# Performance work log

Hardware: AMD Instinct MI355X
Metric: run time of the kernel (lower is better)

## Reference

```python
import jax, jax.numpy as jnp
import numpy as np

EMB = 768
HEADS = 12
HEAD_DIM = EMB // HEADS


def setup_inputs() -> dict:
    key = jax.random.key(0)
    ks = jax.random.split(key, 9)
    B, L, D = 4, 2048, EMB
    s = 1.0 / np.sqrt(D)
    return {
        "x": jax.random.normal(ks[0], (B, L, D), dtype=jnp.float32),
        "Wq": jax.random.normal(ks[1], (D, D), dtype=jnp.float32) * s,
        "bq": jnp.zeros((D,), dtype=jnp.float32),
        "Wk": jax.random.normal(ks[2], (D, D), dtype=jnp.float32) * s,
        "bk": jnp.zeros((D,), dtype=jnp.float32),
        "Wv": jax.random.normal(ks[3], (D, D), dtype=jnp.float32) * s,
        "bv": jnp.zeros((D,), dtype=jnp.float32),
        "Wo": jax.random.normal(ks[4], (D, D), dtype=jnp.float32) * s,
        "bo": jnp.zeros((D,), dtype=jnp.float32),
    }


def reference(x, Wq, bq, Wk, bk, Wv, bv, Wo, bo):
    B, L, D = x.shape
    H, hd = HEADS, HEAD_DIM
    # QKV projections -> [B, H, L, hd]
    def proj(W, b):
        return (x @ W + b).reshape(B, L, H, hd).transpose(0, 2, 1, 3)
    Q = proj(Wq, bq)
    K = proj(Wk, bk)
    V = proj(Wv, bv)
    # scores [B, H, L, L]
    scores = jnp.einsum("bhqd,bhkd->bhqk", Q, K) / jnp.sqrt(jnp.float32(hd))
    attn = jax.nn.softmax(scores, axis=-1)
    out = jnp.einsum("bhqk,bhkd->bhqd", attn, V)  # [B,H,L,hd]
    out = out.transpose(0, 2, 1, 3).reshape(B, L, D)
    return out @ Wo + bo
```

## Files before the change

### kernel.cpp

```cpp
#include <hip/hip_runtime.h>
#include <math.h>

#define TL 2048
#define TD 768
#define NH 12
#define HD 64
#define NB 4
#define MTOT (NB * TL)

typedef __bf16 bf16;
typedef __attribute__((ext_vector_type(4))) __bf16 bf16x4;
typedef __attribute__((ext_vector_type(8))) __bf16 bf16x8;
typedef __attribute__((ext_vector_type(4))) float floatx4;

#define QSCALE 0.18033688011112042f

#define MFMA16(A, B, C) __builtin_amdgcn_mfma_f32_16x16x32_bf16(A, B, C, 0, 0, 0)

__device__ __forceinline__ void gl_lds16(const void* g, void* l) {
    __builtin_amdgcn_global_load_lds(
        (const __attribute__((address_space(1))) void*)g,
        (__attribute__((address_space(3))) void*)l, 16, 0, 0);
}

__device__ __forceinline__ floatx4 exp2x4(floatx4 a) {
    floatx4 r;
    r.x = __builtin_amdgcn_exp2f(a.x);
    r.y = __builtin_amdgcn_exp2f(a.y);
    r.z = __builtin_amdgcn_exp2f(a.z);
    r.w = __builtin_amdgcn_exp2f(a.w);
    return r;
}

__device__ __forceinline__ int kperm(int key) {
    return (key & 35) | ((key >> 2) & 1) << 4 | ((key >> 3) & 3) << 2;
}

__global__ __launch_bounds__(256)
void cast_x_kernel(const float* __restrict__ x, bf16* __restrict__ xb)
{
    size_t i = ((size_t)blockIdx.x * 256 + threadIdx.x) * 4;
    float4 v = *(const float4*)(x + i);
    bf16x4 o;
    o[0] = (bf16)v.x; o[1] = (bf16)v.y; o[2] = (bf16)v.z; o[3] = (bf16)v.w;
    *(bf16x4*)(xb + i) = o;
}

__global__ __launch_bounds__(256)
void transw_kernel(const float* __restrict__ W0, const float* __restrict__ W1,
                   const float* __restrict__ W2, const float* __restrict__ W3,
                   bf16* __restrict__ T0, bf16* __restrict__ T1,
                   bf16* __restrict__ T2, bf16* __restrict__ T3)
{
    const int z = blockIdx.z;
    const float* W = z == 0 ? W0 : z == 1 ? W1 : z == 2 ? W2 : W3;
    bf16*       T = z == 0 ? T0 : z == 1 ? T1 : z == 2 ? T2 : T3;
    __shared__ float Ts[64][65];
    const int t = threadIdx.x;
    const int k0 = blockIdx.x * 64, n0 = blockIdx.y * 64;
    const int rr = t >> 4, cc = (t & 15) * 4;
#pragma unroll
    for (int i = 0; i < 4; ++i) {
        int row = rr + i * 16;
        float4 v = *(const float4*)(W + (size_t)(k0 + row) * TD + n0 + cc);
        Ts[row][cc] = v.x; Ts[row][cc + 1] = v.y;
        Ts[row][cc + 2] = v.z; Ts[row][cc + 3] = v.w;
    }
    __syncthreads();
#pragma unroll
    for (int i = 0; i < 4; ++i) {
        int n = rr + i * 16;
        bf16x4 pk;
#pragma unroll
        for (int j = 0; j < 4; ++j) pk[j] = (bf16)Ts[cc + j][n];
        *(bf16x4*)(T + (size_t)(n0 + n) * TD + k0 + cc) = pk;
    }
}

__global__ __launch_bounds__(256)
void qkv_gemm(const bf16* __restrict__ xb,
              const bf16* __restrict__ Wqt, const bf16* __restrict__ Wkt,
              const bf16* __restrict__ Wvt,
              const float* __restrict__ bq, const float* __restrict__ bk,
              const float* __restrict__ bv,
              bf16* __restrict__ Q, bf16* __restrict__ K, bf16* __restrict__ Vt)
{
    __shared__ __align__(16) bf16 As[128 * 32];
    __shared__ __align__(16) bf16 Bs[128 * 32];
    __shared__ __align__(16) bf16 Eb[4][16 * 72];

    const int t = threadIdx.x;
    const int lane = t & 63, w = t >> 6;
    const int quad = lane >> 4, l16 = lane & 15;
    const int m0 = blockIdx.x * 128;
    const int n0 = blockIdx.y * 128;
    const int which = blockIdx.z;
    const bf16*  W    = which == 0 ? Wqt : which == 1 ? Wkt : Wvt;
    const float* bias = which == 0 ? bq  : which == 1 ? bk  : bv;
    const float scale = which == 0 ? QSCALE : 1.0f;

    const int rm = (w >> 1) * 64, cn = (w & 1) * 64;

    floatx4 acc[4][4];
#pragma unroll
    for (int i = 0; i < 4; ++i)
#pragma unroll
        for (int j = 0; j < 4; ++j) acc[i][j] = (floatx4){0.f, 0.f, 0.f, 0.f};

    const int srow = t >> 2, sseg = (t & 3) * 8;
    const bf16* gA = xb + (size_t)(m0 + srow) * TD + sseg;
    const bf16* gB = W + (size_t)(n0 + srow) * TD + sseg;

    for (int kk = 0; kk < TD; kk += 32) {
        gl_lds16(gA + kk, As + t * 8);
        gl_lds16(gA + kk + (size_t)64 * TD, As + (t + 256) * 8);
        gl_lds16(gB + kk, Bs + t * 8);
        gl_lds16(gB + kk + (size_t)64 * TD, Bs + (t + 256) * 8);
        __syncthreads();
        bf16x8 af[4], bfr[4];
#pragma unroll
        for (int mb = 0; mb < 4; ++mb)
            af[mb] = *(const bf16x8*)&As[(rm + mb * 16 + l16) * 32 + quad * 8];
#pragma unroll
        for (int nb = 0; nb < 4; ++nb)
            bfr[nb] = *(const bf16x8*)&Bs[(cn + nb * 16 + l16) * 32 + quad * 8];
#pragma unroll
        for (int mb = 0; mb < 4; ++mb)
#pragma unroll
            for (int nb = 0; nb < 4; ++nb)
                acc[mb][nb] = MFMA16(af[mb], bfr[nb], acc[mb][nb]);
        __syncthreads();
    }

    float bsc[4];
#pragma unroll
    for (int nb = 0; nb < 4; ++nb)
        bsc[nb] = bias[n0 + cn + nb * 16 + l16] * scale;

    const int token0 = m0 + rm;
    const int b  = token0 >> 11;
    const int l0 = token0 & (TL - 1);
    const int h  = (n0 + cn) >> 6;
    const int bh = b * NH + h;
    bf16* Ew = Eb[w];

    if (which < 2) {
        bf16* gp = (which == 0 ? Q : K) + ((size_t)bh * TL + l0) * HD;
#pragma unroll
        for (int mb = 0; mb < 4; ++mb) {
#pragma unroll
            for (int nb = 0; nb < 4; ++nb)
#pragma unroll
                for (int r = 0; r < 4; ++r)
                    Ew[(quad * 4 + r) * 72 + nb * 16 + l16] =
                        (bf16)(acc[mb][nb][r] * scale + bsc[nb]);
#pragma unroll
            for (int i = 0; i < 2; ++i) {
                int row = i * 8 + (lane >> 3), seg = lane & 7;
                bf16x8 v = *(const bf16x8*)&Ew[row * 72 + seg * 8];
                *(bf16x8*)(gp + (size_t)(mb * 16 + row) * HD + seg * 8) = v;
            }
        }
    } else {
#pragma unroll
        for (int nb = 0; nb < 4; ++nb) {
#pragma unroll
            for (int mb = 0; mb < 4; ++mb) {
                bf16x4 pk;
#pragma unroll
                for (int r = 0; r < 4; ++r) pk[r] = (bf16)(acc[mb][nb][r] + bsc[nb]);
                *(bf16x4*)&Ew[l16 * 72 + mb * 16 + quad * 4] = pk;
            }
#pragma unroll
            for (int i = 0; i < 2; ++i) {
                int row = i * 8 + (lane >> 3), seg = lane & 7;
                bf16x8 v = *(const bf16x8*)&Ew[row * 72 + seg * 8];
                *(bf16x8*)(Vt + ((size_t)bh * HD + nb * 16 + row) * TL + l0 + seg * 8) = v;
            }
        }
    }
}

__global__ __launch_bounds__(256)
void attn_kernel(const bf16* __restrict__ Q, const bf16* __restrict__ K,
                 const bf16* __restrict__ Vt, bf16* __restrict__ O)
{
    __shared__ __align__(16) bf16 Ks[64 * 72];
    __shared__ __align__(16) bf16 Vs[64 * 72];

    const int t = threadIdx.x;
    const int lane = t & 63, w = t >> 6;
    const int quad = lane >> 4, l16 = lane & 15;

    const int n = blockIdx.y * gridDim.x + blockIdx.x;
    const int xcd = n & 7, s = n >> 3;
    const int bh = xcd * 6 + (s >> 4);
    const int q0 = (s & 15) * 128;

    const bf16* Qb = Q + (size_t)bh * TL * HD;
    const bf16* Kb = K + (size_t)bh * TL * HD;
    const bf16* Vb = Vt + (size_t)bh * HD * TL;

    const int qw = q0 + w * 32;
    bf16x8 qf[2][2];
#pragma unroll
    for (int mb = 0; mb < 2; ++mb)
#pragma unroll
        for (int ks = 0; ks < 2; ++ks)
            qf[mb][ks] = *(const bf16x8*)(Qb + (size_t)(qw + mb * 16 + l16) * HD
                                          + ks * 32 + quad * 8);

    float lrow[2] = {0.f, 0.f};
    floatx4 o[2][4];
#pragma unroll
    for (int mb = 0; mb < 2; ++mb)
#pragma unroll
        for (int db = 0; db < 4; ++db) o[mb][db] = (floatx4){0.f, 0.f, 0.f, 0.f};

    const int sr = t >> 3, ss = (t & 7) * 8;
    const int lr0 = kperm(sr), lr1 = kperm(sr + 32);

    for (int kt = 0; kt < TL / 64; ++kt) {
        const int k0 = kt * 64;
        __syncthreads();
        *(float4*)&Ks[lr0 * 72 + ss] = *(const float4*)(Kb + (size_t)(k0 + sr) * HD + ss);
        *(float4*)&Ks[lr1 * 72 + ss] = *(const float4*)(Kb + (size_t)(k0 + sr + 32) * HD + ss);
        *(float4*)&Vs[sr * 72 + ss]  = *(const float4*)(Vb + (size_t)sr * TL + k0 + ss);
        *(float4*)&Vs[(sr + 32) * 72 + ss] = *(const float4*)(Vb + (size_t)(sr + 32) * TL + k0 + ss);
        __syncthreads();

        floatx4 s2[2][4];
#pragma unroll
        for (int nb = 0; nb < 4; ++nb) {
            bf16x8 kf0 = *(const bf16x8*)&Ks[(nb * 16 + l16) * 72 + quad * 8];
            bf16x8 kf1 = *(const bf16x8*)&Ks[(nb * 16 + l16) * 72 + 32 + quad * 8];
#pragma unroll
            for (int mb = 0; mb < 2; ++mb) {
                floatx4 a = (floatx4){0.f, 0.f, 0.f, 0.f};
                a = MFMA16(kf0, qf[mb][0], a);
                a = MFMA16(kf1, qf[mb][1], a);
                s2[mb][nb] = a;
            }
        }

        bf16x8 pA[2][2];
#pragma unroll
        for (int mb = 0; mb < 2; ++mb) {
#pragma unroll
            for (int ks = 0; ks < 2; ++ks) {
                floatx4 p0 = exp2x4(s2[mb][2 * ks]);
                floatx4 p1 = exp2x4(s2[mb][2 * ks + 1]);
                lrow[mb] += (p0.x + p0.y + p0.z + p0.w) + (p1.x + p1.y + p1.z + p1.w);
                bf16x8 pk;
                pk[0] = (bf16)p0.x; pk[1] = (bf16)p0.y; pk[2] = (bf16)p0.z; pk[3] = (bf16)p0.w;
                pk[4] = (bf16)p1.x; pk[5] = (bf16)p1.y; pk[6] = (bf16)p1.z; pk[7] = (bf16)p1.w;
                pA[mb][ks] = pk;
            }
        }

#pragma unroll
        for (int ks = 0; ks < 2; ++ks) {
#pragma unroll
            for (int db = 0; db < 4; ++db) {
                bf16x8 vf = *(const bf16x8*)&Vs[(db * 16 + l16) * 72 + ks * 32 + quad * 8];
#pragma unroll
                for (int mb = 0; mb < 2; ++mb)
                    o[mb][db] = MFMA16(pA[mb][ks], vf, o[mb][db]);
            }
        }
    }

    const int b = bh / NH, h = bh % NH;
#pragma unroll
    for (int mb = 0; mb < 2; ++mb) {
        lrow[mb] += __shfl_xor(lrow[mb], 16);
        lrow[mb] += __shfl_xor(lrow[mb], 32);
        floatx4 inv;
#pragma unroll
        for (int r = 0; r < 4; ++r)
            inv[r] = 1.0f / __shfl(lrow[mb], (lane & 48) | (quad * 4 + r));
#pragma unroll
        for (int db = 0; db < 4; ++db)
#pragma unroll
            for (int r = 0; r < 4; ++r) {
                int l = qw + mb * 16 + quad * 4 + r;
                O[((size_t)b * TL + l) * TD + h * HD + db * 16 + l16] =
                    (bf16)(o[mb][db][r] * inv[r]);
            }
    }
}

__global__ __launch_bounds__(256)
void oproj_gemm(const bf16* __restrict__ A, const bf16* __restrict__ Wt,
                const float* __restrict__ bo, float* __restrict__ out)
{
    __shared__ __align__(16) bf16 As[128 * 32];
    __shared__ __align__(16) bf16 Bs[128 * 32];
    __shared__ __align__(16) float Ef[4][16 * 68];

    const int t = threadIdx.x;
    const int lane = t & 63, w = t >> 6;
    const int quad = lane >> 4, l16 = lane & 15;
    const int m0 = blockIdx.x * 128;
    const int n0 = blockIdx.y * 128;
    const int rm = (w >> 1) * 64, cn = (w & 1) * 64;

    floatx4 acc[4][4];
#pragma unroll
    for (int i = 0; i < 4; ++i)
#pragma unroll
        for (int j = 0; j < 4; ++j) acc[i][j] = (floatx4){0.f, 0.f, 0.f, 0.f};

    const int srow = t >> 2, sseg = (t & 3) * 8;
    const bf16* gA = A + (size_t)(m0 + srow) * TD + sseg;
    const bf16* gB = Wt + (size_t)(n0 + srow) * TD + sseg;

    for (int kk = 0; kk < TD; kk += 32) {
        gl_lds16(gA + kk, As + t * 8);
        gl_lds16(gA + kk + (size_t)64 * TD, As + (t + 256) * 8);
        gl_lds16(gB + kk, Bs + t * 8);
        gl_lds16(gB + kk + (size_t)64 * TD, Bs + (t + 256) * 8);
        __syncthreads();
        bf16x8 af[4], bfr[4];
#pragma unroll
        for (int mb = 0; mb < 4; ++mb)
            af[mb] = *(const bf16x8*)&As[(rm + mb * 16 + l16) * 32 + quad * 8];
#pragma unroll
        for (int nb = 0; nb < 4; ++nb)
            bfr[nb] = *(const bf16x8*)&Bs[(cn + nb * 16 + l16) * 32 + quad * 8];
#pragma unroll
        for (int mb = 0; mb < 4; ++mb)
#pragma unroll
            for (int nb = 0; nb < 4; ++nb)
                acc[mb][nb] = MFMA16(af[mb], bfr[nb], acc[mb][nb]);
        __syncthreads();
    }

    float bb[4];
#pragma unroll
    for (int nb = 0; nb < 4; ++nb) bb[nb] = bo[n0 + cn + nb * 16 + l16];

    float* Ew = Ef[w];
#pragma unroll
    for (int mb = 0; mb < 4; ++mb) {
#pragma unroll
        for (int nb = 0; nb < 4; ++nb)
#pragma unroll
            for (int r = 0; r < 4; ++r)
                Ew[(quad * 4 + r) * 68 + nb * 16 + l16] = acc[mb][nb][r] + bb[nb];
#pragma unroll
        for (int i = 0; i < 4; ++i) {
            int row = i * 4 + (lane >> 4), seg = lane & 15;
            float4 v = *(const float4*)&Ew[row * 68 + seg * 4];
            *(float4*)(out + (size_t)(m0 + rm + mb * 16 + row) * TD + n0 + cn + seg * 4) = v;
        }
    }
}

extern "C" void kernel_launch(void* const* d_in, const int* in_sizes, int n_in,
                              void* d_out, int out_size, void* d_ws, size_t ws_size,
                              hipStream_t stream)
{
    const float* x  = (const float*)d_in[0];
    const float* Wq = (const float*)d_in[1];
    const float* bq = (const float*)d_in[2];
    const float* Wk = (const float*)d_in[3];
    const float* bk = (const float*)d_in[4];
    const float* Wv = (const float*)d_in[5];
    const float* bv = (const float*)d_in[6];
    const float* Wo = (const float*)d_in[7];
    const float* bo = (const float*)d_in[8];

    const size_t NXE = (size_t)MTOT * TD;
    const size_t NWE = (size_t)TD * TD;

    bf16* xb  = (bf16*)d_ws;
    bf16* Wqt = xb + NXE;
    bf16* Wkt = Wqt + NWE;
    bf16* Wvt = Wkt + NWE;
    bf16* Wot = Wvt + NWE;
    bf16* Qb  = Wot + NWE;
    bf16* Kb  = Qb + NXE;
    bf16* Vtb = Kb + NXE;
    bf16* Ob  = Vtb + NXE;

    cast_x_kernel<<<6144, 256, 0, stream>>>(x, xb);
    transw_kernel<<<dim3(12, 12, 4), 256, 0, stream>>>(Wq, Wk, Wv, Wo,
                                                       Wqt, Wkt, Wvt, Wot);
    qkv_gemm<<<dim3(MTOT / 128, TD / 128, 3), 256, 0, stream>>>(
        xb, Wqt, Wkt, Wvt, bq, bk, bv, Qb, Kb, Vtb);
    attn_kernel<<<dim3(TL / 128, NB * NH), 256, 0, stream>>>(Qb, Kb, Vtb, Ob);
    oproj_gemm<<<dim3(MTOT / 128, TD / 128), 256, 0, stream>>>(Ob, Wot, bo,
                                                               (float*)d_out);
}
```

Measured before the change: 218.6 us.

## Use XOR-swizzled LDS layouts with direct global-to-LDS loads and larger K steps

```diff
diff --git a/kernel.cpp b/kernel.cpp
--- a/kernel.cpp
+++ b/kernel.cpp
@@ -32,8 +32,8 @@
     return r;
 }
 
-__device__ __forceinline__ int kperm(int key) {
-    return (key & 35) | ((key >> 2) & 1) << 4 | ((key >> 3) & 3) << 2;
+__device__ __forceinline__ int kperm_inv(int r) {
+    return (r & 35) | (((r >> 2) & 3) << 3) | (((r >> 4) & 1) << 2);
 }
 
 __global__ __launch_bounds__(256)
@@ -85,8 +85,8 @@
               const float* __restrict__ bv,
               bf16* __restrict__ Q, bf16* __restrict__ K, bf16* __restrict__ Vt)
 {
-    __shared__ __align__(16) bf16 As[128 * 32];
-    __shared__ __align__(16) bf16 Bs[128 * 32];
+    __shared__ __align__(16) bf16 As[128 * 64];
+    __shared__ __align__(16) bf16 Bs[128 * 64];
     __shared__ __align__(16) bf16 Eb[4][16 * 72];
 
     const int t = threadIdx.x;
@@ -107,28 +107,41 @@
 #pragma unroll
         for (int j = 0; j < 4; ++j) acc[i][j] = (floatx4){0.f, 0.f, 0.f, 0.f};
 
-    const int srow = t >> 2, sseg = (t & 3) * 8;
-    const bf16* gA = xb + (size_t)(m0 + srow) * TD + sseg;
-    const bf16* gB = W + (size_t)(n0 + srow) * TD + sseg;
-
-    for (int kk = 0; kk < TD; kk += 32) {
-        gl_lds16(gA + kk, As + t * 8);
-        gl_lds16(gA + kk + (size_t)64 * TD, As + (t + 256) * 8);
-        gl_lds16(gB + kk, Bs + t * 8);
-        gl_lds16(gB + kk + (size_t)64 * TD, Bs + (t + 256) * 8);
-        __syncthreads();
-        bf16x8 af[4], bfr[4];
-#pragma unroll
-        for (int mb = 0; mb < 4; ++mb)
-            af[mb] = *(const bf16x8*)&As[(rm + mb * 16 + l16) * 32 + quad * 8];
-#pragma unroll
-        for (int nb = 0; nb < 4; ++nb)
-            bfr[nb] = *(const bf16x8*)&Bs[(cn + nb * 16 + l16) * 32 + quad * 8];
-#pragma unroll
-        for (int mb = 0; mb < 4; ++mb)
-#pragma unroll
-            for (int nb = 0; nb < 4; ++nb)
-                acc[mb][nb] = MFMA16(af[mb], bfr[nb], acc[mb][nb]);
+    const bf16* gA[4];
+    const bf16* gB[4];
+#pragma unroll
+    for (int i = 0; i < 4; ++i) {
+        int n = t + i * 256, r = n >> 3, s = ((n & 7) ^ (r & 7)) * 8;
+        gA[i] = xb + (size_t)(m0 + r) * TD + s;
+        gB[i] = W + (size_t)(n0 + r) * TD + s;
+    }
+
+    for (int kk = 0; kk < TD; kk += 64) {
+#pragma unroll
+        for (int i = 0; i < 4; ++i) {
+            gl_lds16(gA[i] + kk, As + t * 8 + i * 2048);
+            gl_lds16(gB[i] + kk, Bs + t * 8 + i * 2048);
+        }
+        __syncthreads();
+#pragma unroll
+        for (int ks = 0; ks < 2; ++ks) {
+            bf16x8 af[4], bfr[4];
+#pragma unroll
+            for (int mb = 0; mb < 4; ++mb) {
+                int r = rm + mb * 16 + l16;
+                af[mb] = *(const bf16x8*)&As[r * 64 + (((ks * 4 + quad) ^ (r & 7)) * 8)];
+            }
+#pragma unroll
+            for (int nb = 0; nb < 4; ++nb) {
+                int r = cn + nb * 16 + l16;
+                bfr[nb] = *(const bf16x8*)&Bs[r * 64 + (((ks * 4 + quad) ^ (r & 7)) * 8)];
+            }
+#pragma unroll
+            for (int mb = 0; mb < 4; ++mb)
+#pragma unroll
+                for (int nb = 0; nb < 4; ++nb)
+                    acc[mb][nb] = MFMA16(af[mb], bfr[nb], acc[mb][nb]);
+        }
         __syncthreads();
     }
 
@@ -185,8 +198,8 @@
 void attn_kernel(const bf16* __restrict__ Q, const bf16* __restrict__ K,
                  const bf16* __restrict__ Vt, bf16* __restrict__ O)
 {
-    __shared__ __align__(16) bf16 Ks[64 * 72];
-    __shared__ __align__(16) bf16 Vs[64 * 72];
+    __shared__ __align__(16) bf16 Ks[64 * 64];
+    __shared__ __align__(16) bf16 Vs[64 * 64];
 
     const int t = threadIdx.x;
     const int lane = t & 63, w = t >> 6;
@@ -217,23 +230,31 @@
 #pragma unroll
         for (int db = 0; db < 4; ++db) o[mb][db] = (floatx4){0.f, 0.f, 0.f, 0.f};
 
-    const int sr = t >> 3, ss = (t & 7) * 8;
-    const int lr0 = kperm(sr), lr1 = kperm(sr + 32);
+    const bf16* gK[2];
+    const bf16* gV[2];
+#pragma unroll
+    for (int i = 0; i < 2; ++i) {
+        int nn = t + i * 256, r = nn >> 3, sg = ((nn & 7) ^ (r & 7)) * 8;
+        gK[i] = Kb + (size_t)kperm_inv(r) * HD + sg;
+        gV[i] = Vb + (size_t)r * TL + sg;
+    }
 
     for (int kt = 0; kt < TL / 64; ++kt) {
         const int k0 = kt * 64;
         __syncthreads();
-        *(float4*)&Ks[lr0 * 72 + ss] = *(const float4*)(Kb + (size_t)(k0 + sr) * HD + ss);
-        *(float4*)&Ks[lr1 * 72 + ss] = *(const float4*)(Kb + (size_t)(k0 + sr + 32) * HD + ss);
-        *(float4*)&Vs[sr * 72 + ss]  = *(const float4*)(Vb + (size_t)sr * TL + k0 + ss);
-        *(float4*)&Vs[(sr + 32) * 72 + ss] = *(const float4*)(Vb + (size_t)(sr + 32) * TL + k0 + ss);
+#pragma unroll
+        for (int i = 0; i < 2; ++i) {
+            gl_lds16(gK[i] + (size_t)k0 * HD, Ks + t * 8 + i * 2048);
+            gl_lds16(gV[i] + k0,              Vs + t * 8 + i * 2048);
+        }
         __syncthreads();
 
         floatx4 s2[2][4];
 #pragma unroll
         for (int nb = 0; nb < 4; ++nb) {
-            bf16x8 kf0 = *(const bf16x8*)&Ks[(nb * 16 + l16) * 72 + quad * 8];
-            bf16x8 kf1 = *(const bf16x8*)&Ks[(nb * 16 + l16) * 72 + 32 + quad * 8];
+            int r = nb * 16 + l16;
+            bf16x8 kf0 = *(const bf16x8*)&Ks[r * 64 + ((quad ^ (r & 7)) * 8)];
+            bf16x8 kf1 = *(const bf16x8*)&Ks[r * 64 + (((4 + quad) ^ (r & 7)) * 8)];
 #pragma unroll
             for (int mb = 0; mb < 2; ++mb) {
                 floatx4 a = (floatx4){0.f, 0.f, 0.f, 0.f};
@@ -262,7 +283,8 @@
         for (int ks = 0; ks < 2; ++ks) {
 #pragma unroll
             for (int db = 0; db < 4; ++db) {
-                bf16x8 vf = *(const bf16x8*)&Vs[(db * 16 + l16) * 72 + ks * 32 + quad * 8];
+                int r = db * 16 + l16;
+                bf16x8 vf = *(const bf16x8*)&Vs[r * 64 + (((ks * 4 + quad) ^ (r & 7)) * 8)];
 #pragma unroll
                 for (int mb = 0; mb < 2; ++mb)
                     o[mb][db] = MFMA16(pA[mb][ks], vf, o[mb][db]);
@@ -294,8 +316,8 @@
 void oproj_gemm(const bf16* __restrict__ A, const bf16* __restrict__ Wt,
                 const float* __restrict__ bo, float* __restrict__ out)
 {
-    __shared__ __align__(16) bf16 As[128 * 32];
-    __shared__ __align__(16) bf16 Bs[128 * 32];
+    __shared__ __align__(16) bf16 As[128 * 64];
+    __shared__ __align__(16) bf16 Bs[128 * 64];
     __shared__ __align__(16) float Ef[4][16 * 68];
 
     const int t = threadIdx.x;
@@ -311,28 +333,41 @@
 #pragma unroll
         for (int j = 0; j < 4; ++j) acc[i][j] = (floatx4){0.f, 0.f, 0.f, 0.f};
 
-    const int srow = t >> 2, sseg = (t & 3) * 8;
-    const bf16* gA = A + (size_t)(m0 + srow) * TD + sseg;
-    const bf16* gB = Wt + (size_t)(n0 + srow) * TD + sseg;
-
-    for (int kk = 0; kk < TD; kk += 32) {
-        gl_lds16(gA + kk, As + t * 8);
-        gl_lds16(gA + kk + (size_t)64 * TD, As + (t + 256) * 8);
-        gl_lds16(gB + kk, Bs + t * 8);
-        gl_lds16(gB + kk + (size_t)64 * TD, Bs + (t + 256) * 8);
-        __syncthreads();
-        bf16x8 af[4], bfr[4];
-#pragma unroll
-        for (int mb = 0; mb < 4; ++mb)
-            af[mb] = *(const bf16x8*)&As[(rm + mb * 16 + l16) * 32 + quad * 8];
-#pragma unroll
-        for (int nb = 0; nb < 4; ++nb)
-            bfr[nb] = *(const bf16x8*)&Bs[(cn + nb * 16 + l16) * 32 + quad * 8];
-#pragma unroll
-        for (int mb = 0; mb < 4; ++mb)
-#pragma unroll
-            for (int nb = 0; nb < 4; ++nb)
-                acc[mb][nb] = MFMA16(af[mb], bfr[nb], acc[mb][nb]);
+    const bf16* gA[4];
+    const bf16* gB[4];
+#pragma unroll
+    for (int i = 0; i < 4; ++i) {
+        int n = t + i * 256, r = n >> 3, s = ((n & 7) ^ (r & 7)) * 8;
+        gA[i] = A + (size_t)(m0 + r) * TD + s;
+        gB[i] = Wt + (size_t)(n0 + r) * TD + s;
+    }
+
+    for (int kk = 0; kk < TD; kk += 64) {
+#pragma unroll
+        for (int i = 0; i < 4; ++i) {
+            gl_lds16(gA[i] + kk, As + t * 8 + i * 2048);
+            gl_lds16(gB[i] + kk, Bs + t * 8 + i * 2048);
+        }
+        __syncthreads();
+#pragma unroll
+        for (int ks = 0; ks < 2; ++ks) {
+            bf16x8 af[4], bfr[4];
+#pragma unroll
+            for (int mb = 0; mb < 4; ++mb) {
+                int r = rm + mb * 16 + l16;
+                af[mb] = *(const bf16x8*)&As[r * 64 + (((ks * 4 + quad) ^ (r & 7)) * 8)];
+            }
+#pragma unroll
+            for (int nb = 0; nb < 4; ++nb) {
+                int r = cn + nb * 16 + l16;
+                bfr[nb] = *(const bf16x8*)&Bs[r * 64 + (((ks * 4 + quad) ^ (r & 7)) * 8)];
+            }
+#pragma unroll
+            for (int mb = 0; mb < 4; ++mb)
+#pragma unroll
+                for (int nb = 0; nb < 4; ++nb)
+                    acc[mb][nb] = MFMA16(af[mb], bfr[nb], acc[mb][nb]);
+        }
         __syncthreads();
     }
 
```

New measurement: 215.8 us. Within noise of the previous version (-1.3%).
